# Kernel tuning notes

Hardware: AMD Instinct MI355X
Metric: run time of the kernel (lower is better)

## Reference

```python
import jax, jax.numpy as jnp
import numpy as np

D_MODEL = 1024
N_HEAD = 16


def setup_inputs() -> dict:
    key = jax.random.key(0)
    ks = jax.random.split(key, 7)
    B, L, D = 2, 2048, D_MODEL
    s = 0.02
    return {
        "x": jax.random.normal(ks[0], (B, L, D), dtype=jnp.float32),
        "W_kq": jax.random.normal(ks[1], (D, 2 * D), dtype=jnp.float32) * s,
        "b_kq": jax.random.normal(ks[2], (2 * D,), dtype=jnp.float32) * s,
        "W_v": jax.random.normal(ks[3], (D, D), dtype=jnp.float32) * s,
        "b_v": jax.random.normal(ks[4], (D,), dtype=jnp.float32) * s,
        "W_o": jax.random.normal(ks[5], (D, D), dtype=jnp.float32) * s,
        "b_o": jax.random.normal(ks[6], (D,), dtype=jnp.float32) * s,
    }


def reference(x, W_kq, b_kq, W_v, b_v, W_o, b_o):
    B, L, D = x.shape
    H = N_HEAD
    dh = D // H
    kq = x @ W_kq + b_kq            # (B, L, 2D); split order: k first, then q
    k = kq[..., :D].reshape(B, L, H, dh)
    q = kq[..., D:].reshape(B, L, H, dh)
    v = (x @ W_v + b_v).reshape(B, L, H, dh)
    scale = 1.0 / jnp.sqrt(jnp.float32(dh))
    scores = jnp.einsum('blhd,bmhd->bhlm', q, k) * scale  # (B, H, L, L)
    causal = jnp.tril(jnp.ones((L, L), dtype=bool))
    scores = jnp.where(causal, scores, -jnp.inf)
    attn = jax.nn.softmax(scores, axis=-1)
    out = jnp.einsum('bhlm,bmhd->blhd', attn, v).reshape(B, L, D)
    out = out @ W_o + b_o
    return jnp.squeeze(out)
```

## Files before the change

kernel.cpp:

```cpp
#include <hip/hip_runtime.h>
#include <cstdint>


#define LSEQ 2048
#define DM   1024
#define BL   4096

using frag_ab = __attribute__((ext_vector_type(8))) short;
using half8   = __attribute__((ext_vector_type(8))) _Float16;
using half4   = __attribute__((ext_vector_type(4))) _Float16;
using f32x4   = __attribute__((ext_vector_type(4))) float;

__device__ __forceinline__ unsigned short f2bf(float f) {
  unsigned int u = __float_as_uint(f);
  u += 0x7fffu + ((u >> 16) & 1u);
  return (unsigned short)(u >> 16);
}

__device__ __forceinline__ void load_lds16(const void* g, void* l) {
  __builtin_amdgcn_global_load_lds(
      (const __attribute__((address_space(1))) unsigned int*)g,
      (__attribute__((address_space(3))) unsigned int*)l, 16, 0, 0);
}


__global__ __launch_bounds__(256) void prep_kernel(
    const float* __restrict__ x, unsigned short* __restrict__ xb,
    const float* __restrict__ W_kq, const float* __restrict__ W_v,
    const float* __restrict__ W_o,
    unsigned short* __restrict__ wcat, _Float16* __restrict__ wot)
{
  const int bid = blockIdx.x;
  const int tid = threadIdx.x;

  if (bid < 4096) {
    const int i = bid * 256 + tid;
    const float4 v = *(const float4*)&x[(size_t)i * 4];
    ushort4 o;
    o.x = f2bf(v.x); o.y = f2bf(v.y); o.z = f2bf(v.z); o.w = f2bf(v.w);
    *(ushort4*)&xb[(size_t)i * 4] = o;
    return;
  }

  __shared__ float tile[32][33];
  const int r  = tid >> 3;
  const int c4 = (tid & 7) * 4;

  const float* W;
  int N, nb, kb, which;
  if (bid < 6144) {
    const int b2 = bid - 4096;
    W = W_kq; N = 2048; nb = (b2 & 63) * 32; kb = (b2 >> 6) * 32; which = 0;
  } else if (bid < 7168) {
    const int b2 = bid - 6144;
    W = W_v;  N = 1024; nb = (b2 & 31) * 32; kb = (b2 >> 5) * 32; which = 1;
  } else {
    const int b2 = bid - 7168;
    W = W_o;  N = 1024; nb = (b2 & 31) * 32; kb = (b2 >> 5) * 32; which = 2;
  }

  const float4 v = *(const float4*)&W[(size_t)(kb + r) * N + nb + c4];
  tile[r][c4 + 0] = v.x; tile[r][c4 + 1] = v.y;
  tile[r][c4 + 2] = v.z; tile[r][c4 + 3] = v.w;
  __syncthreads();

  if (which == 2) {
    half4 o;
    o[0] = (_Float16)tile[c4 + 0][r];
    o[1] = (_Float16)tile[c4 + 1][r];
    o[2] = (_Float16)tile[c4 + 2][r];
    o[3] = (_Float16)tile[c4 + 3][r];
    *(half4*)&wot[(size_t)(nb + r) * 1024 + kb + c4] = o;
  } else {
    ushort4 o;
    o.x = f2bf(tile[c4 + 0][r]);
    o.y = f2bf(tile[c4 + 1][r]);
    o.z = f2bf(tile[c4 + 2][r]);
    o.w = f2bf(tile[c4 + 3][r]);
    unsigned short* dst = (which == 0) ? wcat : wcat + 2097152;
    *(ushort4*)&dst[(size_t)(nb + r) * 1024 + kb + c4] = o;
  }
}


__global__ __launch_bounds__(256) void gemm_kqv(
    const unsigned short* __restrict__ A, const unsigned short* __restrict__ Bt,
    const float* __restrict__ b_kq, const float* __restrict__ b_v,
    unsigned short* __restrict__ kqb, _Float16* __restrict__ vtb)
{
  const int tid  = threadIdx.x;
  const int lane = tid & 63;
  const int w    = tid >> 6;
  const int wm   = (w >> 1) * 64;
  const int wn   = (w & 1) * 64;
  const int n0   = blockIdx.x * 128;
  const int m0   = blockIdx.y * 128;
  const int quad = lane >> 4;
  const int l15  = lane & 15;
  const int K    = 1024;

  __shared__ __align__(16) unsigned short As[128 * 64];
  __shared__ __align__(16) unsigned short Bs[128 * 64];

  const int srow = lane >> 3;
  const int sc   = (lane & 7) ^ srow;

  const unsigned short* gA = A  + (size_t)(m0 + w * 32 + srow) * K + sc * 8;
  const unsigned short* gB = Bt + (size_t)(n0 + w * 32 + srow) * K + sc * 8;

  f32x4 acc[4][4] = {};

  for (int k0 = 0; k0 < K; k0 += 64) {
    __syncthreads();
#pragma unroll
    for (int i = 0; i < 4; ++i) {
      load_lds16(gA + (size_t)i * 8 * K + k0, &As[(w * 32 + i * 8) * 64 + lane * 8]);
      load_lds16(gB + (size_t)i * 8 * K + k0, &Bs[(w * 32 + i * 8) * 64 + lane * 8]);
    }
    __syncthreads();
#pragma unroll
    for (int kf = 0; kf < 2; ++kf) {
      frag_ab af[4], bf[4];
#pragma unroll
      for (int t = 0; t < 4; ++t) {
        const int ra = wm + t * 16 + l15;
        const int pa = (kf * 4 + quad) ^ (ra & 7);
        af[t] = *(const frag_ab*)&As[ra * 64 + pa * 8];
        const int rb = wn + t * 16 + l15;
        const int pb = (kf * 4 + quad) ^ (rb & 7);
        bf[t] = *(const frag_ab*)&Bs[rb * 64 + pb * 8];
      }
#pragma unroll
      for (int i = 0; i < 4; ++i)
#pragma unroll
        for (int j = 0; j < 4; ++j)
          acc[i][j] = __builtin_amdgcn_mfma_f32_16x16x32_bf16(
              af[i], bf[j], acc[i][j], 0, 0, 0);
    }
  }

  if (n0 >= 2048) {
#pragma unroll
    for (int i = 0; i < 4; ++i)
#pragma unroll
      for (int j = 0; j < 4; ++j) {
        const int row0 = m0 + wm + i * 16 + quad * 4;
        const int col  = n0 - 2048 + wn + j * 16 + l15;
        const float bv = b_v[col];
        half4 pk;
        pk[0] = (_Float16)(acc[i][j][0] + bv);
        pk[1] = (_Float16)(acc[i][j][1] + bv);
        pk[2] = (_Float16)(acc[i][j][2] + bv);
        pk[3] = (_Float16)(acc[i][j][3] + bv);
        *(half4*)&vtb[(size_t)col * BL + row0] = pk;
      }
  } else {
    const float sc2 = (n0 + wn >= 1024) ? 0.125f : 1.0f;
#pragma unroll
    for (int i = 0; i < 4; ++i)
#pragma unroll
      for (int j = 0; j < 4; ++j) {
        const int row0 = m0 + wm + i * 16 + quad * 4;
        const int col  = n0 + wn + j * 16 + l15;
        const float bv = b_kq[col];
#pragma unroll
        for (int r = 0; r < 4; ++r)
          kqb[(size_t)(row0 + r) * 2048 + col] = f2bf((acc[i][j][r] + bv) * sc2);
      }
  }
}


__global__ __launch_bounds__(256, 4) void gemm_out(
    const _Float16* __restrict__ A, const _Float16* __restrict__ Bt,
    const float* __restrict__ bias, float* __restrict__ C)
{
  const int tid  = threadIdx.x;
  const int lane = tid & 63;
  const int w    = tid >> 6;
  const int wm   = (w >> 1) * 64;
  const int wn   = (w & 1) * 32;
  const int n0   = blockIdx.x * 64;
  const int m0   = blockIdx.y * 128;
  const int quad = lane >> 4;
  const int l15  = lane & 15;
  const int K    = 1024;

  __shared__ __align__(16) _Float16 As[128 * 64];
  __shared__ __align__(16) _Float16 Bs[64 * 64];

  const int srow = lane >> 3;
  const int sc   = (lane & 7) ^ srow;

  const _Float16* gA = A  + (size_t)(m0 + w * 32 + srow) * K + sc * 8;
  const _Float16* gB = Bt + (size_t)(n0 + w * 16 + srow) * K + sc * 8;

  f32x4 acc[4][2] = {};

  for (int k0 = 0; k0 < K; k0 += 64) {
    __syncthreads();
#pragma unroll
    for (int i = 0; i < 4; ++i)
      load_lds16(gA + (size_t)i * 8 * K + k0, &As[(w * 32 + i * 8) * 64 + lane * 8]);
#pragma unroll
    for (int i = 0; i < 2; ++i)
      load_lds16(gB + (size_t)i * 8 * K + k0, &Bs[(w * 16 + i * 8) * 64 + lane * 8]);
    __syncthreads();
#pragma unroll
    for (int kf = 0; kf < 2; ++kf) {
      half8 af[4], bf[2];
#pragma unroll
      for (int t = 0; t < 4; ++t) {
        const int ra = wm + t * 16 + l15;
        const int pa = (kf * 4 + quad) ^ (ra & 7);
        af[t] = *(const half8*)&As[ra * 64 + pa * 8];
      }
#pragma unroll
      for (int t = 0; t < 2; ++t) {
        const int rb = wn + t * 16 + l15;
        const int pb = (kf * 4 + quad) ^ (rb & 7);
        bf[t] = *(const half8*)&Bs[rb * 64 + pb * 8];
      }
#pragma unroll
      for (int i = 0; i < 4; ++i)
#pragma unroll
        for (int j = 0; j < 2; ++j)
          acc[i][j] = __builtin_amdgcn_mfma_f32_16x16x32_f16(
              af[i], bf[j], acc[i][j], 0, 0, 0);
    }
  }

#pragma unroll
  for (int i = 0; i < 4; ++i)
#pragma unroll
    for (int j = 0; j < 2; ++j) {
      const int row0 = m0 + wm + i * 16 + quad * 4;
      const int col  = n0 + wn + j * 16 + l15;
      const float bv = bias[col];
#pragma unroll
      for (int r = 0; r < 4; ++r)
        C[(size_t)(row0 + r) * DM + col] = acc[i][j][r] + bv;
    }
}


__global__ __launch_bounds__(256) void attn_mfma(
    const unsigned short* __restrict__ kq, const _Float16* __restrict__ vt,
    _Float16* __restrict__ att)
{
  const int tid  = threadIdx.x;
  const int lane = tid & 63;
  const int w    = tid >> 6;
  const int bx   = blockIdx.x;
  const int qt   = 31 - (bx >> 5);
  const int bh   = bx & 31;
  const int b    = bh >> 4;
  const int h    = bh & 15;
  const int q0   = qt * 64;
  const int quad = lane >> 4;
  const int l15  = lane & 15;

  __shared__ __align__(16) unsigned short Ks[128 * 64];
  __shared__ __align__(16) _Float16      Vs[64 * 128];

#pragma unroll
  for (int i = 0; i < 2; ++i) {
    const int L = i * 256 + tid;
    const int row = L >> 3, c = L & 7;
    const unsigned short* g = kq + (size_t)(b * LSEQ + q0 + row) * 2048
                                 + DM + h * 64 + ((c ^ (row & 7)) * 8);
    load_lds16(g, &Ks[(size_t)L * 8]);
  }
  __syncthreads();
  frag_ab qa[2];
#pragma unroll
  for (int kf = 0; kf < 2; ++kf) {
    const int row = w * 16 + l15;
    const int c = (kf * 4 + quad) ^ (row & 7);
    qa[kf] = *(const frag_ab*)&Ks[row * 64 + c * 8];
  }

  f32x4 oacc[4] = {};
  float mrow = -3e38f, lrow = 0.f;
  const int nk = (qt + 2) >> 1;

  for (int kt = 0; kt < nk; ++kt) {
    const int k0 = kt * 128;
    __syncthreads();
#pragma unroll
    for (int i = 0; i < 4; ++i) {
      const int L = i * 256 + tid;
      {
        const int row = L >> 3, c = L & 7;
        const unsigned short* g = kq + (size_t)(b * LSEQ + k0 + row) * 2048
                                     + h * 64 + ((c ^ (row & 7)) * 8);
        load_lds16(g, &Ks[(size_t)L * 8]);
      }
      {
        const int row = L >> 4, c16 = L & 15;
        const _Float16* g = vt + (size_t)(h * 64 + row) * BL
                               + b * LSEQ + k0 + ((c16 ^ (row & 15)) * 8);
        load_lds16(g, &Vs[(size_t)L * 8]);
      }
    }
    __syncthreads();

    f32x4 st[8];
#pragma unroll
    for (int mt = 0; mt < 8; ++mt) {
      f32x4 s = {};
#pragma unroll
      for (int kf = 0; kf < 2; ++kf) {
        const int row = mt * 16 + l15;
        const int c = (kf * 4 + quad) ^ (row & 7);
        const frag_ab kfrag = *(const frag_ab*)&Ks[row * 64 + c * 8];
        s = __builtin_amdgcn_mfma_f32_16x16x32_bf16(kfrag, qa[kf], s, 0, 0, 0);
      }
      st[mt] = s;
    }

    if (kt == nk - 1) {
      const int qg = q0 + w * 16 + l15;
#pragma unroll
      for (int mt = 0; mt < 8; ++mt)
#pragma unroll
        for (int r = 0; r < 4; ++r)
          if (k0 + mt * 16 + quad * 4 + r > qg) st[mt][r] = -3e38f;
    }

    float mx = -3e38f;
#pragma unroll
    for (int mt = 0; mt < 8; ++mt)
#pragma unroll
      for (int r = 0; r < 4; ++r) mx = fmaxf(mx, st[mt][r]);
    mx = fmaxf(mx, __shfl_xor(mx, 16));
    mx = fmaxf(mx, __shfl_xor(mx, 32));
    const float mnew  = fmaxf(mrow, mx);
    const float alpha = __expf(mrow - mnew);
    half4 pf[8];
    float rsum = 0.f;
#pragma unroll
    for (int mt = 0; mt < 8; ++mt)
#pragma unroll
      for (int r = 0; r < 4; ++r) {
        const float e = __expf(st[mt][r] - mnew);
        rsum += e;
        pf[mt][r] = (_Float16)e;
      }
    rsum += __shfl_xor(rsum, 16);
    rsum += __shfl_xor(rsum, 32);
    lrow = lrow * alpha + rsum;
    mrow = mnew;

    float aq[4];
#pragma unroll
    for (int r = 0; r < 4; ++r) aq[r] = __shfl(alpha, quad * 4 + r);
#pragma unroll
    for (int dt = 0; dt < 4; ++dt)
#pragma unroll
      for (int r = 0; r < 4; ++r) oacc[dt][r] *= aq[r];

#pragma unroll
    for (int c8 = 0; c8 < 8; ++c8) {
#pragma unroll
      for (int dt = 0; dt < 4; ++dt) {
        const int g16 = 2 * c8 + (quad >> 1);
        const half4 vf = *(const half4*)&Vs[(dt * 16 + l15) * 128
                                            + ((g16 ^ l15) << 3) + ((quad & 1) << 2)];
        oacc[dt] = __builtin_amdgcn_mfma_f32_16x16x16f16(pf[c8], vf, oacc[dt], 0, 0, 0);
      }
    }
  }

  float lq[4];
#pragma unroll
  for (int r = 0; r < 4; ++r) lq[r] = 1.0f / __shfl(lrow, quad * 4 + r);
#pragma unroll
  for (int dt = 0; dt < 4; ++dt)
#pragma unroll
    for (int r = 0; r < 4; ++r) {
      const int row = b * LSEQ + q0 + w * 16 + quad * 4 + r;
      const int col = h * 64 + dt * 16 + l15;
      att[(size_t)row * DM + col] = (_Float16)(oacc[dt][r] * lq[r]);
    }
}


extern "C" void kernel_launch(void* const* d_in, const int* in_sizes, int n_in,
                              void* d_out, int out_size, void* d_ws, size_t ws_size,
                              hipStream_t stream)
{
  const float* x    = (const float*)d_in[0];
  const float* W_kq = (const float*)d_in[1];
  const float* b_kq = (const float*)d_in[2];
  const float* W_v  = (const float*)d_in[3];
  const float* b_v  = (const float*)d_in[4];
  const float* W_o  = (const float*)d_in[5];
  const float* b_o  = (const float*)d_in[6];

  unsigned short* ws   = (unsigned short*)d_ws;
  unsigned short* xb   = ws;
  unsigned short* wcat = xb   + 4194304;
  _Float16*       wot  = (_Float16*)(wcat + 3145728);
  unsigned short* kqb  = (unsigned short*)(wot + 1048576);
  _Float16*       vtb  = (_Float16*)(kqb + 8388608);
  _Float16*       attb = vtb + 4194304;

  prep_kernel<<<8192, 256, 0, stream>>>(x, xb, W_kq, W_v, W_o, wcat, wot);
  gemm_kqv<<<dim3(24, 32), 256, 0, stream>>>(xb, wcat, b_kq, b_v, kqb, vtb);
  attn_mfma<<<1024, 256, 0, stream>>>(kqb, vtb, attb);
  gemm_out<<<dim3(16, 32), 256, 0, stream>>>(attb, wot, b_o, (float*)d_out);
}
```

Measured before the change: 187.1 us.

## Split long causal query tiles across two blocks and merge partial softmax results

The longest query tiles (qt 20-31) are split into two key-range chunks, each computed by a separate block that writes unnormalized partial outputs plus running max and sum. A new merge kernel combines them, so the attention grid grows from 1024 to 1408 blocks and work per block is more even across the causal triangle. The query scale is folded with log2(e) so the kernel can use exp2f instead of __expf. In exchange it adds an extra kernel launch and fp32 partial traffic. The partial buffers reuse the start of the workspace, which also holds the converted x and weights that are already consumed by then.

```diff
diff --git a/kernel.cpp b/kernel.cpp
--- a/kernel.cpp
+++ b/kernel.cpp
@@ -155,7 +155,7 @@
         *(half4*)&vtb[(size_t)col * BL + row0] = pk;
       }
   } else {
-    const float sc2 = (n0 + wn >= 1024) ? 0.125f : 1.0f;
+    const float sc2 = (n0 + wn >= 1024) ? 0.18033688011112042f : 1.0f;
 #pragma unroll
     for (int i = 0; i < 4; ++i)
 #pragma unroll
@@ -246,19 +246,37 @@
 
 __global__ __launch_bounds__(256) void attn_mfma(
     const unsigned short* __restrict__ kq, const _Float16* __restrict__ vt,
-    _Float16* __restrict__ att)
+    _Float16* __restrict__ att,
+    float* __restrict__ Opart, float* __restrict__ mlpart)
 {
   const int tid  = threadIdx.x;
   const int lane = tid & 63;
   const int w    = tid >> 6;
   const int bx   = blockIdx.x;
-  const int qt   = 31 - (bx >> 5);
+  const int j    = bx >> 5;
   const int bh   = bx & 31;
   const int b    = bh >> 4;
   const int h    = bh & 15;
-  const int q0   = qt * 64;
   const int quad = lane >> 4;
   const int l15  = lane & 15;
+
+  int qt, kt0, kt1, pt = -1;
+  if (j < 2) {
+    qt = 19 - j; kt0 = 0; kt1 = (qt + 2) >> 1;
+  } else if (j < 26) {
+    const int qq = j - 2;
+    qt = 31 - (qq >> 1);
+    const int chunk = qq & 1;
+    const int nkk = (qt + 2) >> 1;
+    const int nh  = nkk >> 1;
+    kt0 = chunk ? nh : 0;
+    kt1 = chunk ? nkk : nh;
+    pt  = ((31 - qt) * 2 + chunk) * 32 + bh;
+  } else {
+    qt = 43 - j; kt0 = 0; kt1 = (qt + 2) >> 1;
+  }
+  const int q0 = qt * 64;
+  const int nk = (qt + 2) >> 1;
 
   __shared__ __align__(16) unsigned short Ks[128 * 64];
   __shared__ __align__(16) _Float16      Vs[64 * 128];
@@ -282,9 +300,8 @@
 
   f32x4 oacc[4] = {};
   float mrow = -3e38f, lrow = 0.f;
-  const int nk = (qt + 2) >> 1;
-
-  for (int kt = 0; kt < nk; ++kt) {
+
+  for (int kt = kt0; kt < kt1; ++kt) {
     const int k0 = kt * 128;
     __syncthreads();
 #pragma unroll
@@ -336,14 +353,14 @@
     mx = fmaxf(mx, __shfl_xor(mx, 16));
     mx = fmaxf(mx, __shfl_xor(mx, 32));
     const float mnew  = fmaxf(mrow, mx);
-    const float alpha = __expf(mrow - mnew);
+    const float alpha = exp2f(mrow - mnew);
     half4 pf[8];
     float rsum = 0.f;
 #pragma unroll
     for (int mt = 0; mt < 8; ++mt)
 #pragma unroll
       for (int r = 0; r < 4; ++r) {
-        const float e = __expf(st[mt][r] - mnew);
+        const float e = exp2f(st[mt][r] - mnew);
         rsum += e;
         pf[mt][r] = (_Float16)e;
       }
@@ -372,17 +389,77 @@
     }
   }
 
-  float lq[4];
-#pragma unroll
-  for (int r = 0; r < 4; ++r) lq[r] = 1.0f / __shfl(lrow, quad * 4 + r);
-#pragma unroll
-  for (int dt = 0; dt < 4; ++dt)
-#pragma unroll
-    for (int r = 0; r < 4; ++r) {
-      const int row = b * LSEQ + q0 + w * 16 + quad * 4 + r;
-      const int col = h * 64 + dt * 16 + l15;
-      att[(size_t)row * DM + col] = (_Float16)(oacc[dt][r] * lq[r]);
-    }
+  if (pt < 0) {
+    float lq[4];
+#pragma unroll
+    for (int r = 0; r < 4; ++r) lq[r] = 1.0f / __shfl(lrow, quad * 4 + r);
+#pragma unroll
+    for (int dt = 0; dt < 4; ++dt)
+#pragma unroll
+      for (int r = 0; r < 4; ++r) {
+        const int row = b * LSEQ + q0 + w * 16 + quad * 4 + r;
+        const int col = h * 64 + dt * 16 + l15;
+        att[(size_t)row * DM + col] = (_Float16)(oacc[dt][r] * lq[r]);
+      }
+  } else {
+    if (quad == 0) {
+      mlpart[(size_t)pt * 128 + w * 16 + l15]      = mrow;
+      mlpart[(size_t)pt * 128 + 64 + w * 16 + l15] = lrow;
+    }
+#pragma unroll
+    for (int dt = 0; dt < 4; ++dt)
+#pragma unroll
+      for (int r = 0; r < 4; ++r) {
+        const int row = w * 16 + quad * 4 + r;
+        const int col = dt * 16 + l15;
+        Opart[(size_t)pt * 4096 + row * 64 + col] = oacc[dt][r];
+      }
+  }
+}
+
+
+__global__ __launch_bounds__(256) void attn_merge(
+    const float* __restrict__ Opart, const float* __restrict__ mlpart,
+    _Float16* __restrict__ att)
+{
+  const int t   = blockIdx.x;
+  const int s   = t >> 5;
+  const int bh  = t & 31;
+  const int qt  = 31 - s;
+  const int b   = bh >> 4;
+  const int h   = bh & 15;
+  const int q0  = qt * 64;
+  const int p0  = (s * 2 + 0) * 32 + bh;
+  const int p1  = (s * 2 + 1) * 32 + bh;
+  const int tid = threadIdx.x;
+  const int row = tid >> 2;
+  const int c0  = (tid & 3) * 16;
+
+  const float m1 = mlpart[(size_t)p0 * 128 + row];
+  const float l1 = mlpart[(size_t)p0 * 128 + 64 + row];
+  const float m2 = mlpart[(size_t)p1 * 128 + row];
+  const float l2 = mlpart[(size_t)p1 * 128 + 64 + row];
+  const float m  = fmaxf(m1, m2);
+  const float e1 = exp2f(m1 - m);
+  const float e2 = exp2f(m2 - m);
+  const float inv = 1.0f / (e1 * l1 + e2 * l2);
+  const float f1 = e1 * inv, f2 = e2 * inv;
+
+  const float* O1 = Opart + (size_t)p0 * 4096 + row * 64 + c0;
+  const float* O2 = Opart + (size_t)p1 * 4096 + row * 64 + c0;
+  _Float16*   dst = att + (size_t)(b * LSEQ + q0 + row) * DM + h * 64 + c0;
+
+#pragma unroll
+  for (int i = 0; i < 4; ++i) {
+    const float4 a = *(const float4*)&O1[i * 4];
+    const float4 c = *(const float4*)&O2[i * 4];
+    half4 o;
+    o[0] = (_Float16)(f1 * a.x + f2 * c.x);
+    o[1] = (_Float16)(f1 * a.y + f2 * c.y);
+    o[2] = (_Float16)(f1 * a.z + f2 * c.z);
+    o[3] = (_Float16)(f1 * a.w + f2 * c.w);
+    *(half4*)&dst[i * 4] = o;
+  }
 }
 
 
@@ -406,8 +483,12 @@
   _Float16*       vtb  = (_Float16*)(kqb + 8388608);
   _Float16*       attb = vtb + 4194304;
 
+  float* Opart  = (float*)ws;
+  float* mlpart = Opart + 768 * 4096;
+
   prep_kernel<<<8192, 256, 0, stream>>>(x, xb, W_kq, W_v, W_o, wcat, wot);
   gemm_kqv<<<dim3(24, 32), 256, 0, stream>>>(xb, wcat, b_kq, b_v, kqb, vtb);
-  attn_mfma<<<1024, 256, 0, stream>>>(kqb, vtb, attb);
+  attn_mfma<<<1408, 256, 0, stream>>>(kqb, vtb, attb, Opart, mlpart);
+  attn_merge<<<384, 256, 0, stream>>>(Opart, mlpart, attb);
   gemm_out<<<dim3(16, 32), 256, 0, stream>>>(attb, wot, b_o, (float*)d_out);
 }
```

Result: slower. 195.4 us (+4.5%).

## Pipeline K/V tile loads and use exp2 softmax with lazy rescaling

Applied to the files above, without the earlier changes.

The attention loop now issues the next K tile's loads after the QK^T MFMAs and the next V tile's loads after the PV MFMAs. Hand-placed s_waitcnt/s_barrier pairs replace __syncthreads so global-to-LDS transfers overlap compute. The Q scale now folds in log2(e) so softmax can use exp2 directly. The running-max rescale is skipped when the max grows by at most 8, and probabilities are packed with cvt_pkrtz. This adds hand-counted vmcnt dependencies and some fp16 overflow risk from the lazy-rescale threshold.

```diff
diff --git a/kernel.cpp b/kernel.cpp
--- a/kernel.cpp
+++ b/kernel.cpp
@@ -9,12 +9,19 @@
 using frag_ab = __attribute__((ext_vector_type(8))) short;
 using half8   = __attribute__((ext_vector_type(8))) _Float16;
 using half4   = __attribute__((ext_vector_type(4))) _Float16;
+using half2_t = __attribute__((ext_vector_type(2))) _Float16;
+using fp16x2  = __attribute__((ext_vector_type(2))) __fp16;
 using f32x4   = __attribute__((ext_vector_type(4))) float;
 
 __device__ __forceinline__ unsigned short f2bf(float f) {
   unsigned int u = __float_as_uint(f);
   u += 0x7fffu + ((u >> 16) & 1u);
   return (unsigned short)(u >> 16);
+}
+
+__device__ __forceinline__ half2_t pkrtz(float a, float b) {
+  const fp16x2 r = __builtin_amdgcn_cvt_pkrtz(a, b);
+  return __builtin_bit_cast(half2_t, r);
 }
 
 __device__ __forceinline__ void load_lds16(const void* g, void* l) {
@@ -155,7 +162,7 @@
         *(half4*)&vtb[(size_t)col * BL + row0] = pk;
       }
   } else {
-    const float sc2 = (n0 + wn >= 1024) ? 0.125f : 1.0f;
+    const float sc2 = (n0 + wn >= 1024) ? 0.18033688011112042f : 1.0f;
 #pragma unroll
     for (int i = 0; i < 4; ++i)
 #pragma unroll
@@ -271,7 +278,7 @@
                                  + DM + h * 64 + ((c ^ (row & 7)) * 8);
     load_lds16(g, &Ks[(size_t)L * 8]);
   }
-  __syncthreads();
+  asm volatile("s_waitcnt vmcnt(0)\n\ts_barrier" ::: "memory");
   frag_ab qa[2];
 #pragma unroll
   for (int kf = 0; kf < 2; ++kf) {
@@ -279,31 +286,44 @@
     const int c = (kf * 4 + quad) ^ (row & 7);
     qa[kf] = *(const frag_ab*)&Ks[row * 64 + c * 8];
   }
+  asm volatile("s_waitcnt lgkmcnt(0)\n\ts_barrier" ::: "memory");
+
+  const int nk = (qt + 2) >> 1;
+
+#define STAGE_K(K0)                                                            \
+  {                                                                            \
+    _Pragma("unroll")                                                          \
+    for (int i = 0; i < 4; ++i) {                                              \
+      const int L = i * 256 + tid;                                             \
+      const int row = L >> 3, c = L & 7;                                       \
+      const unsigned short* g = kq + (size_t)(b * LSEQ + (K0) + row) * 2048    \
+                                   + h * 64 + ((c ^ (row & 7)) * 8);           \
+      load_lds16(g, &Ks[(size_t)L * 8]);                                       \
+    }                                                                          \
+  }
+#define STAGE_V(K0)                                                            \
+  {                                                                            \
+    _Pragma("unroll")                                                          \
+    for (int i = 0; i < 4; ++i) {                                              \
+      const int L = i * 256 + tid;                                             \
+      const int row = L >> 4, c16 = L & 15;                                    \
+      const _Float16* g = vt + (size_t)(h * 64 + row) * BL                     \
+                             + b * LSEQ + (K0) + ((c16 ^ (row & 15)) * 8);     \
+      load_lds16(g, &Vs[(size_t)L * 8]);                                       \
+    }                                                                          \
+  }
+
+  STAGE_K(0);
+  STAGE_V(0);
 
   f32x4 oacc[4] = {};
   float mrow = -3e38f, lrow = 0.f;
-  const int nk = (qt + 2) >> 1;
 
   for (int kt = 0; kt < nk; ++kt) {
     const int k0 = kt * 128;
-    __syncthreads();
-#pragma unroll
-    for (int i = 0; i < 4; ++i) {
-      const int L = i * 256 + tid;
-      {
-        const int row = L >> 3, c = L & 7;
-        const unsigned short* g = kq + (size_t)(b * LSEQ + k0 + row) * 2048
-                                     + h * 64 + ((c ^ (row & 7)) * 8);
-        load_lds16(g, &Ks[(size_t)L * 8]);
-      }
-      {
-        const int row = L >> 4, c16 = L & 15;
-        const _Float16* g = vt + (size_t)(h * 64 + row) * BL
-                               + b * LSEQ + k0 + ((c16 ^ (row & 15)) * 8);
-        load_lds16(g, &Vs[(size_t)L * 8]);
-      }
-    }
-    __syncthreads();
+    const bool more = (kt + 1 < nk);
+
+    asm volatile("s_waitcnt vmcnt(4)\n\ts_barrier" ::: "memory");
 
     f32x4 st[8];
 #pragma unroll
@@ -319,6 +339,9 @@
       st[mt] = s;
     }
 
+    asm volatile("s_waitcnt lgkmcnt(0)\n\ts_barrier" ::: "memory");
+    if (more) STAGE_K(k0 + 128);
+
     if (kt == nk - 1) {
       const int qg = q0 + w * 16 + l15;
 #pragma unroll
@@ -328,37 +351,55 @@
           if (k0 + mt * 16 + quad * 4 + r > qg) st[mt][r] = -3e38f;
     }
 
-    float mx = -3e38f;
-#pragma unroll
-    for (int mt = 0; mt < 8; ++mt)
-#pragma unroll
-      for (int r = 0; r < 4; ++r) mx = fmaxf(mx, st[mt][r]);
+    float mx = fmaxf(st[0][0], st[0][1]);
+    mx = fmaxf(fmaxf(mx, st[0][2]), st[0][3]);
+#pragma unroll
+    for (int mt = 1; mt < 8; ++mt) {
+      mx = fmaxf(fmaxf(mx, st[mt][0]), st[mt][1]);
+      mx = fmaxf(fmaxf(mx, st[mt][2]), st[mt][3]);
+    }
     mx = fmaxf(mx, __shfl_xor(mx, 16));
     mx = fmaxf(mx, __shfl_xor(mx, 32));
-    const float mnew  = fmaxf(mrow, mx);
-    const float alpha = __expf(mrow - mnew);
+
+    if (!__all(mx - mrow <= 8.0f)) {
+      const float mnew  = fmaxf(mrow, mx);
+      const float alpha = __builtin_amdgcn_exp2f(mrow - mnew);
+      float aq[4];
+#pragma unroll
+      for (int r = 0; r < 4; ++r) aq[r] = __shfl(alpha, quad * 4 + r);
+#pragma unroll
+      for (int dt = 0; dt < 4; ++dt)
+#pragma unroll
+        for (int r = 0; r < 4; ++r) oacc[dt][r] *= aq[r];
+      lrow *= alpha;
+      mrow = mnew;
+    }
+
     half4 pf[8];
-    float rsum = 0.f;
-#pragma unroll
-    for (int mt = 0; mt < 8; ++mt)
-#pragma unroll
-      for (int r = 0; r < 4; ++r) {
-        const float e = __expf(st[mt][r] - mnew);
-        rsum += e;
-        pf[mt][r] = (_Float16)e;
-      }
+    float rs0 = 0.f, rs1 = 0.f, rs2 = 0.f, rs3 = 0.f;
+#pragma unroll
+    for (int mt = 0; mt < 8; ++mt) {
+      const float e0 = __builtin_amdgcn_exp2f(st[mt][0] - mrow);
+      const float e1 = __builtin_amdgcn_exp2f(st[mt][1] - mrow);
+      const float e2 = __builtin_amdgcn_exp2f(st[mt][2] - mrow);
+      const float e3 = __builtin_amdgcn_exp2f(st[mt][3] - mrow);
+      rs0 += e0; rs1 += e1; rs2 += e2; rs3 += e3;
+      const half2_t p01 = pkrtz(e0, e1);
+      const half2_t p23 = pkrtz(e2, e3);
+      half4 p;
+      p[0] = p01[0]; p[1] = p01[1]; p[2] = p23[0]; p[3] = p23[1];
+      pf[mt] = p;
+    }
+    float rsum = (rs0 + rs1) + (rs2 + rs3);
     rsum += __shfl_xor(rsum, 16);
     rsum += __shfl_xor(rsum, 32);
-    lrow = lrow * alpha + rsum;
-    mrow = mnew;
-
-    float aq[4];
-#pragma unroll
-    for (int r = 0; r < 4; ++r) aq[r] = __shfl(alpha, quad * 4 + r);
-#pragma unroll
-    for (int dt = 0; dt < 4; ++dt)
-#pragma unroll
-      for (int r = 0; r < 4; ++r) oacc[dt][r] *= aq[r];
+    lrow += rsum;
+
+    if (more) {
+      asm volatile("s_waitcnt vmcnt(4)\n\ts_barrier" ::: "memory");
+    } else {
+      asm volatile("s_waitcnt vmcnt(0)\n\ts_barrier" ::: "memory");
+    }
 
 #pragma unroll
     for (int c8 = 0; c8 < 8; ++c8) {
@@ -370,6 +411,11 @@
         oacc[dt] = __builtin_amdgcn_mfma_f32_16x16x16f16(pf[c8], vf, oacc[dt], 0, 0, 0);
       }
     }
+
+    if (more) {
+      asm volatile("s_waitcnt lgkmcnt(0)\n\ts_barrier" ::: "memory");
+      STAGE_V(k0 + 128);
+    }
   }
 
   float lq[4];
@@ -383,6 +429,8 @@
       const int col = h * 64 + dt * 16 + l15;
       att[(size_t)row * DM + col] = (_Float16)(oacc[dt][r] * lq[r]);
     }
+#undef STAGE_K
+#undef STAGE_V
 }
 
 
```

After: 183.7 us. No clear change (-1.8%).
